# Kernel optimization log

Hardware: AMD Instinct MI355X
Metric: run time of the kernel (lower is better)

Reference implementation:

```python
import jax, jax.numpy as jnp
import numpy as np

N = 50000      # nodes
E = 100000     # edges
D_IN = 16      # raw node feature dim
K = 16         # RWSE steps
H = 32         # node_hidden_dim (== D_IN + K for residual)
ED = H * H     # edge_input_dim, must be H*H for NNConv reshape


def _seg_sum(x, idx, n):
    return jax.ops.segment_sum(x, idx, num_segments=n)


def setup_inputs() -> dict:
    key = jax.random.key(0)
    ks = jax.random.split(key, 14)
    s = 0.02
    return {
        "n_feat": jax.random.normal(ks[0], (N, D_IN), jnp.float32),
        "e_feat": jax.random.normal(ks[1], (E, ED), jnp.float32),
        "src": jax.random.randint(ks[2], (E,), 0, N, jnp.int32),
        "dst": jax.random.randint(ks[3], (E,), 0, N, jnp.int32),
        "edge_proj_w": jax.random.normal(ks[4], (ED, ED), jnp.float32) * s,
        "edge_proj_b": jnp.zeros((ED,), jnp.float32),
        "gate_w": jax.random.normal(ks[5], (ED, 1), jnp.float32) * s,
        "gate_b": jnp.zeros((1,), jnp.float32),
        "lin0_w": jax.random.normal(ks[6], (D_IN + K, H), jnp.float32) * s,
        "lin0_b": jnp.zeros((H,), jnp.float32),
        "conv_bias": jnp.zeros((H,), jnp.float32),
        "message_w": jax.random.normal(ks[7], (2 * H, H), jnp.float32) * s,
        "message_b": jnp.zeros((H,), jnp.float32),
        "subgraph_w": jax.random.normal(ks[8], (2 * H, H), jnp.float32) * s,
        "subgraph_b": jnp.zeros((H,), jnp.float32),
    }


def reference(n_feat, e_feat, src, dst, edge_proj_w, edge_proj_b, gate_w, gate_b,
              lin0_w, lin0_b, conv_bias, message_w, message_b, subgraph_w, subgraph_b):
    ones_e = jnp.ones((E,), n_feat.dtype)
    deg = _seg_sum(ones_e, dst, N)                 # in-degree (adj row-sum)
    degc = jnp.where(deg == 0, 1.0, deg)

    # --- RWSE (sparse equivalent of dense adj @ x recursion) ---
    x = degc
    cols = [x]
    for _ in range(K - 1):
        x = _seg_sum(x[src], dst, N) / degc
        cols.append(x)
    rwse = jnp.stack(cols, axis=1)                 # (N, K)

    nf = jnp.concatenate([n_feat, rwse], axis=-1)  # (N, D_IN+K)
    init = nf
    out = jax.nn.relu(nf @ lin0_w + lin0_b)        # (N, H)

    # --- edge-conditioned weights (EnhancedEdgeNetwork), same every step ---
    proj = jax.nn.relu(e_feat @ edge_proj_w + edge_proj_b)   # (E, H*H)
    gate = jax.nn.sigmoid(e_feat @ gate_w + gate_b)          # (E, 1)
    W = (proj * gate).reshape(E, H, H)                       # (E, H, H)

    # --- NNConv mean-aggregation message passing (num_steps//2 iters) ---
    for _ in range(3):
        msg = jnp.einsum('eh,eho->eo', out[src], W)          # gather + transform
        neigh = _seg_sum(msg, dst, N) / degc[:, None]        # scatter-mean
        m = jax.nn.relu(neigh + out + conv_bias)             # residual (identity) + bias
        out = jnp.concatenate([m, out], axis=1) @ message_w + message_b

    # --- copy_u/mean group pooling + subgraph projection ---
    group = _seg_sum(out[src], dst, N) / degc[:, None]
    out = jnp.concatenate([out, group], axis=1) @ subgraph_w + subgraph_b
    return out + init
```

## Files before the change

### kernel.cpp

```cpp
#include <hip/hip_runtime.h>
#include <hip/hip_bf16.h>

typedef unsigned short u16;
typedef unsigned int   u32;
typedef __bf16 bf16x8 __attribute__((ext_vector_type(8)));
typedef float  f32x4  __attribute__((ext_vector_type(4)));

#define AS1 __attribute__((address_space(1)))
#define AS3 __attribute__((address_space(3)))

__device__ __forceinline__ u16 f2bf(float f){
    u32 u = __float_as_uint(f);
    u32 r = u + 0x7fffu + ((u>>16)&1u);
    return (u16)(r>>16);
}
__device__ __forceinline__ float bf2f(u16 u){ return __uint_as_float(((u32)u)<<16); }

__global__ void k_deg(const int* __restrict__ dst, float* __restrict__ degb, int E){
    int e = blockIdx.x*256 + threadIdx.x;
    if (e < E) atomicAdd(&degb[dst[e]], 1.0f);
}

__global__ void k_degc(float* __restrict__ invdeg, float* __restrict__ rw0, int n){
    int v = blockIdx.x*256 + threadIdx.x;
    if (v < n){
        float c = invdeg[v];
        if (c == 0.f) c = 1.f;
        invdeg[v] = 1.f/c;
        rw0[v] = c*c;
    }
}

__global__ void k_rwse(const float* __restrict__ cur, float* __restrict__ nxt,
                       const float* __restrict__ invdeg, const int* __restrict__ src,
                       const int* __restrict__ dst, int E){
    int e = blockIdx.x*256 + threadIdx.x;
    if (e < E){
        int s = src[e];
        atomicAdd(&nxt[dst[e]], cur[s]*invdeg[s]);
    }
}

__global__ void k_finalize(const float* __restrict__ nfeat, const float* __restrict__ rw,
                           const float* __restrict__ invdeg,
                           const float* __restrict__ lw, const float* __restrict__ lb,
                           float* __restrict__ out0, int n){
    __shared__ float lwl[1024];
    __shared__ float lbl[32];
    __shared__ float nfl[8][32];
    int tid = threadIdx.x;
    for (int i = tid; i < 1024; i += 256) lwl[i] = lw[i];
    if (tid < 32) lbl[tid] = lb[tid];
    int slot = tid>>5, o = tid&31;
    int v = blockIdx.x*8 + slot;
    float nfv = 0.f;
    if (v < n){
        nfv = (o < 16) ? nfeat[(size_t)v*16 + o]
                       : rw[(size_t)(o-16)*n + v]*invdeg[v];
    }
    nfl[slot][o] = nfv;
    __syncthreads();
    if (v < n){
        float a = lbl[o];
        #pragma unroll
        for (int j = 0; j < 32; j++) a += nfl[slot][j]*lwl[j*32+o];
        out0[(size_t)v*32 + o] = a > 0.f ? a : 0.f;
    }
}

__global__ void k_transpose(const float* __restrict__ w, u16* __restrict__ wt){
    __shared__ float t[32][33];
    int bx = blockIdx.x & 31, by = blockIdx.x >> 5;
    int x = threadIdx.x & 31, y = threadIdx.x >> 5;
    #pragma unroll
    for (int i = 0; i < 32; i += 8)
        t[y+i][x] = w[(size_t)(by*32 + y + i)*1024 + bx*32 + x];
    __syncthreads();
    #pragma unroll
    for (int i = 0; i < 32; i += 8)
        wt[(size_t)(bx*32 + y + i)*1024 + by*32 + x] = f2bf(t[x][y+i]);
}

__global__ __launch_bounds__(256) void k_prep(
    const float* __restrict__ A, const float* __restrict__ gw,
    const float* __restrict__ gb, u16* __restrict__ Abf,
    float* __restrict__ gate, int E)
{
    __shared__ f32x4 gwl[256];
    const int tid = threadIdx.x;
    const int wave = tid>>6, lane = tid&63;
    gwl[tid] = ((const f32x4*)gw)[tid];
    __syncthreads();
    const int row = blockIdx.x*4 + wave;
    if (row >= E) return;
    const f32x4* ar = (const f32x4*)(A + (size_t)row*1024);
    ushort4* br = (ushort4*)(Abf + (size_t)row*1024);
    float g = 0.f;
    #pragma unroll
    for (int j = 0; j < 4; j++){
        const int idx = j*64 + lane;
        f32x4 v = ar[idx];
        f32x4 w4 = gwl[idx];
        g += v.x*w4.x + v.y*w4.y + v.z*w4.z + v.w*w4.w;
        ushort4 o;
        o.x = f2bf(v.x); o.y = f2bf(v.y); o.z = f2bf(v.z); o.w = f2bf(v.w);
        br[idx] = o;
    }
    #pragma unroll
    for (int m = 32; m >= 1; m >>= 1) g += __shfl_xor(g, m);
    if (lane == 0) gate[row] = 1.f/(1.f + __expf(-(g + gb[0])));
}

__global__ __launch_bounds__(256) void k_gemm(
    const u16* __restrict__ A, const u16* __restrict__ BT,
    const float* __restrict__ bias, const float* __restrict__ gate,
    u16* __restrict__ Wout, int E)
{
    __shared__ __align__(16) u16 lds_a[128*32];
    __shared__ __align__(16) u16 lds_b[128*32];
    __shared__ float gate_lds[128];
    __shared__ float bias_lds[128];

    const int tid  = threadIdx.x;
    const int wave = tid>>6, lane = tid&63;
    const int wm = wave>>1, wn = wave&1;
    const int ql = lane>>4, rl = lane&15;

    const int id  = blockIdx.x;
    const int xcd = id & 7;
    const int s   = id >> 3;
    const int nb  = s & 7;
    const int mb  = (s >> 3)*8 + xcd;
    const int MBtot = (E + 127) >> 7;
    if (mb >= MBtot) return;
    const int m0 = mb<<7, n0 = nb<<7;

    if (tid < 128){
        const int row = m0 + tid;
        gate_lds[tid] = gate[row < E ? row : E-1];
    } else {
        bias_lds[tid-128] = bias[n0 + tid - 128];
    }

    f32x4 acc[4][4];
    #pragma unroll
    for (int i=0;i<4;i++)
    #pragma unroll
        for (int j=0;j<4;j++) acc[i][j] = (f32x4){0.f,0.f,0.f,0.f};

    for (int k0 = 0; k0 < 1024; k0 += 32){
        __syncthreads();
        #pragma unroll
        for (int j=0;j<2;j++){
            const int cb = (j*4 + wave)*64;
            const int ci = cb + lane;
            const int m  = ci & 127, q = ci >> 7;
            int row = m0 + m; if (row >= E) row = E-1;
            const u16* ga = A + (size_t)row*1024 + k0 + q*8;
            __builtin_amdgcn_global_load_lds(
                (const AS1 void*)ga, (AS3 void*)&lds_a[ci*8], 16, 0, 0);
            const u16* gB = BT + (size_t)(n0 + m)*1024 + (k0 + q*8);
            __builtin_amdgcn_global_load_lds(
                (const AS1 void*)gB, (AS3 void*)&lds_b[ci*8], 16, 0, 0);
        }
        __syncthreads();

        bf16x8 af[4], bfr[4];
        #pragma unroll
        for (int t=0;t<4;t++){
            af[t]  = *(const bf16x8*)&lds_a[(ql*128 + wm*64 + t*16 + rl)*8];
            bfr[t] = *(const bf16x8*)&lds_b[(ql*128 + wn*64 + t*16 + rl)*8];
        }
        #pragma unroll
        for (int mt=0;mt<4;mt++)
        #pragma unroll
            for (int nt=0;nt<4;nt++)
                acc[mt][nt] = __builtin_amdgcn_mfma_f32_16x16x32_bf16(af[mt], bfr[nt], acc[mt][nt], 0,0,0);
    }

    float bcol[4];
    #pragma unroll
    for (int nt=0;nt<4;nt++) bcol[nt] = bias_lds[wn*64 + nt*16 + rl];

    #pragma unroll
    for (int mt=0;mt<4;mt++){
        const int rloc0 = wm*64 + mt*16 + ql*4;
        #pragma unroll
        for (int r=0;r<4;r++){
            const int row = m0 + rloc0 + r;
            if (row < E){
                const float g = gate_lds[rloc0 + r];
                u16* wrow = Wout + (size_t)row*1024 + n0 + wn*64 + rl;
                #pragma unroll
                for (int nt=0;nt<4;nt++){
                    float v = acc[mt][nt][r] + bcol[nt];
                    v = v > 0.f ? v : 0.f;
                    wrow[nt*16] = f2bf(v*g);
                }
            }
        }
    }
}

__global__ void k_msg(const float* __restrict__ outc, const u16* __restrict__ W,
                      const int* __restrict__ src, const int* __restrict__ dst,
                      float* __restrict__ neigh, int E)
{
    __shared__ float xl[8][32];
    const int tid = threadIdx.x, slot = tid>>5, o = tid&31;
    const int e = blockIdx.x*8 + slot;
    int d = 0;
    if (e < E){
        d = dst[e];
        xl[slot][o] = outc[(size_t)src[e]*32 + o];
    }
    __syncthreads();
    if (e < E){
        const float* x = xl[slot];
        const u16* wr = W + (size_t)e*1024 + o;
        float acc = 0.f;
        #pragma unroll
        for (int h = 0; h < 32; h++)
            acc += x[h]*bf2f(wr[h*32]);
        atomicAdd(&neigh[(size_t)d*32 + o], acc);
    }
}

__global__ void k_node(const float* __restrict__ neigh, const float* __restrict__ invdeg,
                       const float* __restrict__ outc, const float* __restrict__ cb,
                       const float* __restrict__ mw, const float* __restrict__ mb,
                       float* __restrict__ outn, int n)
{
    __shared__ float mwl[2048];
    __shared__ float cat[8][64];
    int tid = threadIdx.x;
    for (int i = tid; i < 2048; i += 256) mwl[i] = mw[i];
    int slot = tid>>5, o = tid&31;
    int v = blockIdx.x*8 + slot;
    if (v < n){
        float ov = outc[(size_t)v*32 + o];
        float m = neigh[(size_t)v*32 + o]*invdeg[v] + ov + cb[o];
        m = m > 0.f ? m : 0.f;
        cat[slot][o] = m;
        cat[slot][32+o] = ov;
    }
    __syncthreads();
    if (v < n){
        float a = mb[o];
        #pragma unroll
        for (int j = 0; j < 64; j++) a += cat[slot][j]*mwl[j*32+o];
        outn[(size_t)v*32 + o] = a;
    }
}

__global__ void k_group(const float* __restrict__ outc, const int* __restrict__ src,
                        const int* __restrict__ dst, float* __restrict__ grp, int E)
{
    int tid = threadIdx.x, slot = tid>>5, o = tid&31;
    int e = blockIdx.x*8 + slot;
    if (e < E)
        atomicAdd(&grp[(size_t)dst[e]*32 + o], outc[(size_t)src[e]*32 + o]);
}

__global__ void k_final(const float* __restrict__ outc, const float* __restrict__ grp,
                        const float* __restrict__ invdeg, const float* __restrict__ sw,
                        const float* __restrict__ sb, const float* __restrict__ nfeat,
                        const float* __restrict__ rw,
                        float* __restrict__ dout, int n)
{
    __shared__ float swl[2048];
    __shared__ float cat[8][64];
    int tid = threadIdx.x;
    for (int i = tid; i < 2048; i += 256) swl[i] = sw[i];
    int slot = tid>>5, o = tid&31;
    int v = blockIdx.x*8 + slot;
    float iv = 0.f;
    if (v < n){
        iv = invdeg[v];
        cat[slot][o] = outc[(size_t)v*32 + o];
        cat[slot][32+o] = grp[(size_t)v*32 + o]*iv;
    }
    __syncthreads();
    if (v < n){
        float a = sb[o];
        #pragma unroll
        for (int j = 0; j < 64; j++) a += cat[slot][j]*swl[j*32+o];
        float initv = (o < 16) ? nfeat[(size_t)v*16 + o]
                               : rw[(size_t)(o-16)*n + v]*iv;
        dout[(size_t)v*32 + o] = a + initv;
    }
}

extern "C" void kernel_launch(void* const* d_in, const int* in_sizes, int n_in,
                              void* d_out, int out_size, void* d_ws, size_t ws_size,
                              hipStream_t stream)
{
    const float* n_feat = (const float*)d_in[0];
    const float* e_feat = (const float*)d_in[1];
    const int*   src    = (const int*)d_in[2];
    const int*   dst    = (const int*)d_in[3];
    const float* epw    = (const float*)d_in[4];
    const float* epb    = (const float*)d_in[5];
    const float* gw     = (const float*)d_in[6];
    const float* gb     = (const float*)d_in[7];
    const float* l0w    = (const float*)d_in[8];
    const float* l0b    = (const float*)d_in[9];
    const float* cb     = (const float*)d_in[10];
    const float* mw     = (const float*)d_in[11];
    const float* mbp    = (const float*)d_in[12];
    const float* sw     = (const float*)d_in[13];
    const float* sb     = (const float*)d_in[14];

    const int N = in_sizes[0] / 16;
    const int E = in_sizes[2];

    char* w = (char*)d_ws;
    float* invdeg = (float*)w;  w += (size_t)N*4;
    float* rw     = (float*)w;  w += (size_t)16*N*4;
    float* out_a  = (float*)w;  w += (size_t)32*N*4;
    float* out_b  = (float*)w;  w += (size_t)32*N*4;
    float* neigh  = (float*)w;  w += (size_t)32*N*4;
    u16*   wtb    = (u16*)w;    w += (size_t)1024*1024*2;
    u16*   abf    = (u16*)w;    w += (size_t)E*1024*2;
    float* gatev  = (float*)w;  w += (size_t)E*4;
    u16*   wout   = (u16*)w;

    hipMemsetAsync(invdeg, 0, (size_t)N*4, stream);
    hipMemsetAsync(rw, 0, (size_t)16*N*4, stream);

    const int EB  = (E + 255)/256, NB = (N + 255)/256;
    const int EB8 = (E + 7)/8,    NB8 = (N + 7)/8;

    k_deg<<<EB,256,0,stream>>>(dst, invdeg, E);
    k_degc<<<NB,256,0,stream>>>(invdeg, rw, N);
    for (int t = 0; t < 15; t++)
        k_rwse<<<EB,256,0,stream>>>(rw + (size_t)t*N, rw + (size_t)(t+1)*N, invdeg, src, dst, E);
    k_finalize<<<NB8,256,0,stream>>>(n_feat, rw, invdeg, l0w, l0b, out_a, N);

    k_transpose<<<1024,256,0,stream>>>(epw, wtb);
    k_prep<<<(E+3)/4,256,0,stream>>>(e_feat, gw, gb, abf, gatev, E);

    const int MBtot = (E + 127)/128;
    const int grid  = ((MBtot + 7)/8)*64;
    k_gemm<<<grid,256,0,stream>>>(abf, wtb, epb, gatev, wout, E);

    float* cur = out_a; float* nxt = out_b;
    for (int it = 0; it < 3; it++){
        hipMemsetAsync(neigh, 0, (size_t)32*N*4, stream);
        k_msg<<<EB8,256,0,stream>>>(cur, wout, src, dst, neigh, E);
        k_node<<<NB8,256,0,stream>>>(neigh, invdeg, cur, cb, mw, mbp, nxt, N);
        float* tmp = cur; cur = nxt; nxt = tmp;
    }

    hipMemsetAsync(neigh, 0, (size_t)32*N*4, stream);
    k_group<<<EB8,256,0,stream>>>(cur, src, dst, neigh, E);
    k_final<<<NB8,256,0,stream>>>(cur, neigh, invdeg, sw, sb, n_feat, rw, (float*)d_out, N);

    (void)n_in; (void)out_size; (void)ws_size;
}
```

Baseline: 1.420 ms.

## Triple-buffer LDS tiles in edge GEMM to overlap global loads with MFMA

The edge-projection GEMM now keeps three LDS stages for the A and B tiles. It issues global-to-LDS loads two k-steps ahead and uses explicit vmcnt waits with a single barrier per iteration in place of two __syncthreads. This is meant to hide global memory latency behind the MFMA work, which the old load-sync-compute loop left exposed. It triples the LDS use for the tiles, which can lower occupancy, and its correctness depends on the hand-written waitcnt counts.

```diff
diff --git a/kernel.cpp b/kernel.cpp
--- a/kernel.cpp
+++ b/kernel.cpp
@@ -116,8 +116,8 @@
     const float* __restrict__ bias, const float* __restrict__ gate,
     u16* __restrict__ Wout, int E)
 {
-    __shared__ __align__(16) u16 lds_a[128*32];
-    __shared__ __align__(16) u16 lds_b[128*32];
+    __shared__ __align__(16) u16 lds_a[3*128*32];
+    __shared__ __align__(16) u16 lds_b[3*128*32];
     __shared__ float gate_lds[128];
     __shared__ float bias_lds[128];
 
@@ -141,6 +141,25 @@
     } else {
         bias_lds[tid-128] = bias[n0 + tid - 128];
     }
+    __syncthreads();
+
+#define STAGE(buf, kk)                                                      \
+    {                                                                       \
+        const int k0s = (kk);                                               \
+        _Pragma("unroll")                                                   \
+        for (int j=0;j<2;j++){                                              \
+            const int cb = (j*4 + wave)*64;                                 \
+            const int ci = cb + lane;                                       \
+            const int m  = ci & 127, q = ci >> 7;                           \
+            int row = m0 + m; if (row >= E) row = E-1;                      \
+            const u16* ga = A + (size_t)row*1024 + k0s + q*8;               \
+            __builtin_amdgcn_global_load_lds((const AS1 void*)ga,           \
+                (AS3 void*)&lds_a[(buf)*4096 + ci*8], 16, 0, 0);            \
+            const u16* gB = BT + (size_t)(n0 + m)*1024 + (k0s + q*8);       \
+            __builtin_amdgcn_global_load_lds((const AS1 void*)gB,           \
+                (AS3 void*)&lds_b[(buf)*4096 + ci*8], 16, 0, 0);            \
+        }                                                                   \
+    }
 
     f32x4 acc[4][4];
     #pragma unroll
@@ -148,35 +167,39 @@
     #pragma unroll
         for (int j=0;j<4;j++) acc[i][j] = (f32x4){0.f,0.f,0.f,0.f};
 
-    for (int k0 = 0; k0 < 1024; k0 += 32){
-        __syncthreads();
-        #pragma unroll
-        for (int j=0;j<2;j++){
-            const int cb = (j*4 + wave)*64;
-            const int ci = cb + lane;
-            const int m  = ci & 127, q = ci >> 7;
-            int row = m0 + m; if (row >= E) row = E-1;
-            const u16* ga = A + (size_t)row*1024 + k0 + q*8;
-            __builtin_amdgcn_global_load_lds(
-                (const AS1 void*)ga, (AS3 void*)&lds_a[ci*8], 16, 0, 0);
-            const u16* gB = BT + (size_t)(n0 + m)*1024 + (k0 + q*8);
-            __builtin_amdgcn_global_load_lds(
-                (const AS1 void*)gB, (AS3 void*)&lds_b[ci*8], 16, 0, 0);
+    STAGE(0, 0)
+    STAGE(1, 32)
+    asm volatile("s_waitcnt vmcnt(4)" ::: "memory");
+    __builtin_amdgcn_s_barrier();
+
+    int bc = 0;
+    for (int t = 0; t < 32; ++t){
+        if (t + 2 < 32){
+            int bs = bc + 2; if (bs >= 3) bs -= 3;
+            STAGE(bs, (t+2)*32)
         }
-        __syncthreads();
-
+
+        const u16* la = &lds_a[bc*4096];
+        const u16* lb = &lds_b[bc*4096];
         bf16x8 af[4], bfr[4];
         #pragma unroll
-        for (int t=0;t<4;t++){
-            af[t]  = *(const bf16x8*)&lds_a[(ql*128 + wm*64 + t*16 + rl)*8];
-            bfr[t] = *(const bf16x8*)&lds_b[(ql*128 + wn*64 + t*16 + rl)*8];
+        for (int tt=0;tt<4;tt++){
+            af[tt]  = *(const bf16x8*)&la[(ql*128 + wm*64 + tt*16 + rl)*8];
+            bfr[tt] = *(const bf16x8*)&lb[(ql*128 + wn*64 + tt*16 + rl)*8];
         }
         #pragma unroll
         for (int mt=0;mt<4;mt++)
         #pragma unroll
             for (int nt=0;nt<4;nt++)
                 acc[mt][nt] = __builtin_amdgcn_mfma_f32_16x16x32_bf16(af[mt], bfr[nt], acc[mt][nt], 0,0,0);
-    }
+
+        if (t + 2 < 32)      asm volatile("s_waitcnt vmcnt(4)" ::: "memory");
+        else if (t + 1 < 32) asm volatile("s_waitcnt vmcnt(0)" ::: "memory");
+        if (t + 1 < 32) __builtin_amdgcn_s_barrier();
+
+        bc = bc + 1; if (bc >= 3) bc -= 3;
+    }
+#undef STAGE
 
     float bcol[4];
     #pragma unroll
```

New measurement: 1.415 ms. About the same (-0.4%).
